# Kernel tuning notes

Measured on AMD Instinct MI355X. Metric: run time of the kernel, lower is better.

## Reference

```python
import jax, jax.numpy as jnp
import numpy as np

SOS_TOKEN = 0
VOCAB, EMBED, HIDDEN = 32000, 256, 256


def setup_inputs() -> dict:
    key = jax.random.key(0)
    ks = jax.random.split(key, 10)
    B, S, T = 32, 128, 128
    s = 0.05
    return {
        "encoder_outputs": jax.random.normal(ks[0], (B, S, HIDDEN), jnp.float32),
        "encoder_hidden": jax.random.normal(ks[1], (1, B, HIDDEN), jnp.float32),
        "target_tensor": jax.random.randint(ks[2], (B, T), 0, VOCAB),
        "embedding": jax.random.normal(ks[3], (VOCAB, EMBED), jnp.float32) * s,
        "W_ih": jax.random.normal(ks[4], (3 * HIDDEN, EMBED + HIDDEN), jnp.float32) * s,
        "W_hh": jax.random.normal(ks[5], (3 * HIDDEN, HIDDEN), jnp.float32) * s,
        "b_ih": jax.random.normal(ks[6], (3 * HIDDEN,), jnp.float32) * s,
        "b_hh": jax.random.normal(ks[7], (3 * HIDDEN,), jnp.float32) * s,
        "W_out": jax.random.normal(ks[8], (VOCAB, HIDDEN), jnp.float32) * s,
        "b_out": jax.random.normal(ks[9], (VOCAB,), jnp.float32) * s,
    }


def _decode(encoder_outputs, encoder_hidden, target_tensor, embedding,
            W_ih, W_hh, b_ih, b_hh, W_out, b_out):
    B, T = target_tensor.shape
    # full teacher forcing: decoder input at step t is target[t-1], step 0 is SOS
    dec_in = jnp.concatenate(
        [jnp.full((B, 1), SOS_TOKEN, dtype=target_tensor.dtype), target_tensor[:, :-1]], axis=1)
    emb = embedding[dec_in]                                     # (B,T,E)
    # attention: query = embedded input, key = value = encoder_outputs
    scores = jnp.einsum("bte,bse->bts", emb, encoder_outputs)   # (B,T,S)
    attn = jax.nn.softmax(scores, axis=2)
    context = jnp.einsum("bts,bsh->bth", attn, encoder_outputs)  # (B,T,H)
    x_seq = jnp.concatenate([emb, context], axis=2)             # (B,T,E+H)
    x_seq = jnp.swapaxes(x_seq, 0, 1)                           # (T,B,E+H)

    def gru_step(h, x):
        gi = x @ W_ih.T + b_ih                                  # (B,3H)
        gh = h @ W_hh.T + b_hh
        i_r, i_z, i_n = jnp.split(gi, 3, axis=1)
        h_r, h_z, h_n = jnp.split(gh, 3, axis=1)
        r = jax.nn.sigmoid(i_r + h_r)
        z = jax.nn.sigmoid(i_z + h_z)
        n = jnp.tanh(i_n + r * h_n)
        h_new = (1.0 - z) * n + z * h
        return h_new, h_new

    h0 = encoder_hidden[0]                                      # (B,H)
    _, hs = jax.lax.scan(gru_step, h0, x_seq)                   # (T,B,H)
    logits = hs @ W_out.T + b_out                               # (T,B,V)
    return jnp.swapaxes(logits, 0, 1)                           # (B,T,V)


def reference(encoder_outputs, encoder_hidden, target_tensor, embedding,
              W_ih, W_hh, b_ih, b_hh, W_out, b_out):
    return _decode(encoder_outputs, encoder_hidden, target_tensor, embedding,
                   W_ih, W_hh, b_ih, b_hh, W_out, b_out)
```

## Files before the change

kernel.cpp:

```cpp
#include <hip/hip_runtime.h>
#include <hip/hip_bf16.h>
#include <stdint.h>

typedef float    f32x4  __attribute__((ext_vector_type(4)));
typedef __bf16   bf16x8 __attribute__((ext_vector_type(8)));
typedef _Float16 f16x8  __attribute__((ext_vector_type(8)));
typedef _Float16 h2v    __attribute__((ext_vector_type(2)));

#define B_ 32
#define S_ 128
#define T_ 128
#define H_ 256
#define E_ 256
#define V_ 32000

__device__ __forceinline__ void gll16(const void* g, void* l) {
  __builtin_amdgcn_global_load_lds(
      (const __attribute__((address_space(1))) uint32_t*)g,
      (__attribute__((address_space(3))) uint32_t*)l,
      16, 0, 0);
}

__device__ __forceinline__ uint32_t pack_pair(float a, float b) {
  unsigned short lo = __builtin_bit_cast(unsigned short, (_Float16)a);
  unsigned short hi = __builtin_bit_cast(unsigned short, (_Float16)b);
  return (uint32_t)lo | ((uint32_t)hi << 16);
}

__device__ __forceinline__ uint32_t pack_bf16(float a, float b) {
  return (uint32_t)__builtin_bit_cast(unsigned short, __float2bfloat16(a)) |
         ((uint32_t)__builtin_bit_cast(unsigned short, __float2bfloat16(b)) << 16);
}

__device__ __forceinline__ float dot2(uint32_t w, uint32_t h, float acc) {
#if __has_builtin(__builtin_amdgcn_fdot2)
  return __builtin_amdgcn_fdot2(__builtin_bit_cast(h2v, w),
                                __builtin_bit_cast(h2v, h), acc, false);
#else
  h2v wv = __builtin_bit_cast(h2v, w);
  h2v hv = __builtin_bit_cast(h2v, h);
  return acc + (float)wv.x * (float)hv.x + (float)wv.y * (float)hv.y;
#endif
}

__device__ __forceinline__ float sigmoid_fast(float x) {
  return __fdividef(1.f, 1.f + __expf(-x));
}
__device__ __forceinline__ float tanh_fast(float x) {
  float e = __expf(2.f * fabsf(x));
  float t = 1.f - __fdividef(2.f, e + 1.f);
  return copysignf(t, x);
}

__global__ __launch_bounds__(256) void cvt_bf16_kernel(
    const float* __restrict__ src, uint32_t* __restrict__ dst, int n) {
  int i = (blockIdx.x * 256 + threadIdx.x) * 8;
  if (i + 7 < n) {
    float4 a = *(const float4*)(src + i);
    float4 b = *(const float4*)(src + i + 4);
    uint4 o;
    o.x = pack_bf16(a.x, a.y);
    o.y = pack_bf16(a.z, a.w);
    o.z = pack_bf16(b.x, b.y);
    o.w = pack_bf16(b.z, b.w);
    *(uint4*)(dst + (i >> 1)) = o;
  }
}

__global__ __launch_bounds__(256) void cvt_f16_kernel(
    const float* __restrict__ src, uint32_t* __restrict__ dst, int n) {
  int i = (blockIdx.x * 256 + threadIdx.x) * 4;
  if (i + 3 < n) {
    float4 v = *(const float4*)(src + i);
    uint2 p;
    p.x = pack_pair(v.x, v.y);
    p.y = pack_pair(v.z, v.w);
    *(uint2*)(dst + (i >> 1)) = p;
  }
}

__global__ __launch_bounds__(256) void pack_whh(
    const float* __restrict__ Whh, uint32_t* __restrict__ Wp) {
  __shared__ float lds[32][257];
  int j0 = blockIdx.x * 32;
  int tid = threadIdx.x;
  #pragma unroll 4
  for (int i = 0; i < 32; ++i)
    lds[i][tid] = Whh[(size_t)(j0 + i) * 256 + tid];
  __syncthreads();
  #pragma unroll 4
  for (int i = 0; i < 16; ++i) {
    int e = i * 256 + tid;
    int k2 = e >> 5;
    int jj = e & 31;
    Wp[(size_t)k2 * 768 + j0 + jj] = pack_pair(lds[jj][2 * k2], lds[jj][2 * k2 + 1]);
  }
}

__global__ __launch_bounds__(256) void attn_kernel(
    const float* __restrict__ enc,
    const int*   __restrict__ tgt,
    const float* __restrict__ embt,
    uint32_t*    __restrict__ xh)
{
  int b   = blockIdx.x;
  int tc  = blockIdx.y;
  int tid = threadIdx.x;
  __shared__ __align__(16) float e_sh[256];
  __shared__ float attn_sh[128];
  __shared__ float red_sh[4];
  const float* encb = enc + (size_t)b * S_ * H_;

  for (int tt = 0; tt < 8; ++tt) {
    int t = tc * 8 + tt;
    int tok = (t == 0) ? 0 : tgt[b * T_ + t - 1];
    float ev = embt[(size_t)tok * E_ + tid];
    e_sh[tid] = ev;
    {
      float other = __shfl_xor(ev, 1);
      if (!(tid & 1))
        xh[(size_t)(t * B_ + b) * 256 + (tid >> 1)] = pack_pair(ev, other);
    }
    __syncthreads();

    float sc = 0.f;
    if (tid < 128) {
      const float* er = encb + tid * H_;
      #pragma unroll 8
      for (int k = 0; k < 256; k += 4) {
        float4 e4 = *(const float4*)(e_sh + k);
        float4 r4 = *(const float4*)(er + k);
        sc += e4.x * r4.x; sc += e4.y * r4.y; sc += e4.z * r4.z; sc += e4.w * r4.w;
      }
      float mx = sc;
      #pragma unroll
      for (int o = 32; o > 0; o >>= 1) mx = fmaxf(mx, __shfl_xor(mx, o, 64));
      if ((tid & 63) == 0) red_sh[tid >> 6] = mx;
    }
    __syncthreads();
    float gmax = fmaxf(red_sh[0], red_sh[1]);
    float p = 0.f;
    if (tid < 128) {
      p = __expf(sc - gmax);
      float s = p;
      #pragma unroll
      for (int o = 32; o > 0; o >>= 1) s += __shfl_xor(s, o, 64);
      if ((tid & 63) == 0) red_sh[2 + (tid >> 6)] = s;
    }
    __syncthreads();
    float tot = red_sh[2] + red_sh[3];
    if (tid < 128) attn_sh[tid] = p / tot;
    __syncthreads();

    float ctx = 0.f;
    #pragma unroll 4
    for (int s = 0; s < 128; ++s) ctx += attn_sh[s] * encb[s * H_ + tid];
    {
      float other = __shfl_xor(ctx, 1);
      if (!(tid & 1))
        xh[(size_t)(t * B_ + b) * 256 + 128 + (tid >> 1)] = pack_pair(ctx, other);
    }
    __syncthreads();
  }
}

__global__ __launch_bounds__(256) void gi_gemm_f16(
    const _Float16* __restrict__ A,
    const _Float16* __restrict__ Bm,
    const float* __restrict__ bih,
    float* __restrict__ gi)
{
  __shared__ _Float16 sA[128 * 64];
  __shared__ _Float16 sB[128 * 64];
  int tid = threadIdx.x;
  int n0 = blockIdx.x * 128;
  int m0 = blockIdx.y * 128;
  int lane = tid & 63;
  int wave = tid >> 6;
  int wm = (wave >> 1) * 64;
  int wn = (wave & 1) * 64;
  int srow = tid >> 3;
  int sk   = (tid & 7) * 8;
  f32x4 acc[4][4] = {};

  for (int kt = 0; kt < 512; kt += 64) {
    #pragma unroll
    for (int it = 0; it < 4; ++it) {
      int row = it * 32 + srow;
      gll16(A  + (size_t)(m0 + row) * 512 + kt + sk, &sA[row * 64 + sk]);
      gll16(Bm + (size_t)(n0 + row) * 512 + kt + sk, &sB[row * 64 + sk]);
    }
    __syncthreads();
    #pragma unroll
    for (int kk = 0; kk < 2; ++kk) {
      f16x8 af[4], bfr[4];
      #pragma unroll
      for (int m = 0; m < 4; ++m)
        af[m] = *(const f16x8*)&sA[(wm + m * 16 + (lane & 15)) * 64 + kk * 32 + (lane >> 4) * 8];
      #pragma unroll
      for (int n = 0; n < 4; ++n)
        bfr[n] = *(const f16x8*)&sB[(wn + n * 16 + (lane & 15)) * 64 + kk * 32 + (lane >> 4) * 8];
      #pragma unroll
      for (int m = 0; m < 4; ++m)
        #pragma unroll
        for (int n = 0; n < 4; ++n)
          acc[m][n] = __builtin_amdgcn_mfma_f32_16x16x32_f16(af[m], bfr[n], acc[m][n], 0, 0, 0);
    }
    __syncthreads();
  }

  #pragma unroll
  for (int n = 0; n < 4; ++n) {
    int col = n0 + wn + n * 16 + (lane & 15);
    float bv = bih[col];
    #pragma unroll
    for (int m = 0; m < 4; ++m) {
      int rbase = m0 + wm + m * 16 + (lane >> 4) * 4;
      #pragma unroll
      for (int r = 0; r < 4; ++r)
        gi[(size_t)(rbase + r) * 768 + col] = acc[m][n][r] + bv;
    }
  }
}

__global__ __launch_bounds__(768) void gru_kernel(
    const float*    __restrict__ gi,
    const uint32_t* __restrict__ Wp,
    const float*    __restrict__ bhh,
    const float*    __restrict__ h0,
    __hip_bfloat16* __restrict__ hs)
{
  int b   = blockIdx.x;
  int tid = threadIdx.x;
  int role = tid >> 8;
  int j    = tid & 255;
  __shared__ __align__(16) uint32_t h2[128];
  __shared__ float r_sh[256];
  __shared__ float z_sh[256];

  uint32_t w[128];
  #pragma unroll
  for (int i = 0; i < 128; ++i) w[i] = Wp[(size_t)i * 768 + tid];
  float bj = bhh[tid];

  float hprev = 0.f;
  if (role == 2) {
    hprev = h0[b * 256 + j];
    float other = __shfl_xor(hprev, 1);
    if (!(j & 1)) h2[j >> 1] = pack_pair(hprev, other);
  }
  float gval = gi[(size_t)b * 768 + tid];
  __syncthreads();

  for (int t = 0; t < 128; ++t) {
    float gnext = 0.f;
    if (t < 127) gnext = gi[(size_t)((t + 1) * 32 + b) * 768 + tid];

    float a0 = 0.f, a1 = 0.f, a2 = 0.f, a3 = 0.f;
    float a4 = 0.f, a5 = 0.f, a6 = 0.f, a7 = 0.f;
    #pragma unroll
    for (int k8 = 0; k8 < 16; ++k8) {
      uint4 ha = *(const uint4*)&h2[k8 * 8];
      uint4 hb = *(const uint4*)&h2[k8 * 8 + 4];
      a0 = dot2(w[k8 * 8 + 0], ha.x, a0);
      a1 = dot2(w[k8 * 8 + 1], ha.y, a1);
      a2 = dot2(w[k8 * 8 + 2], ha.z, a2);
      a3 = dot2(w[k8 * 8 + 3], ha.w, a3);
      a4 = dot2(w[k8 * 8 + 4], hb.x, a4);
      a5 = dot2(w[k8 * 8 + 5], hb.y, a5);
      a6 = dot2(w[k8 * 8 + 6], hb.z, a6);
      a7 = dot2(w[k8 * 8 + 7], hb.w, a7);
    }
    float gh = ((a0 + a1) + (a2 + a3)) + ((a4 + a5) + (a6 + a7)) + bj;

    if (role == 0)      r_sh[j] = sigmoid_fast(gval + gh);
    else if (role == 1) z_sh[j] = sigmoid_fast(gval + gh);
    __syncthreads();

    if (role == 2) {
      float r = r_sh[j];
      float z = z_sh[j];
      float n = tanh_fast(gval + r * gh);
      float hn = (1.f - z) * n + z * hprev;
      hprev = hn;
      hs[(size_t)(t * 32 + b) * 256 + j] = __float2bfloat16(hn);
      float other = __shfl_xor(hn, 1);
      if (!(j & 1)) h2[j >> 1] = pack_pair(hn, other);
    }
    gval = gnext;
    __syncthreads();
  }
}

__global__ __launch_bounds__(256) void logits_gemm(
    const __hip_bfloat16* __restrict__ A,
    const __hip_bfloat16* __restrict__ Bm,
    const float* __restrict__ bout,
    float* __restrict__ out)
{
  __shared__ __hip_bfloat16 sA[128 * 64];
  __shared__ __hip_bfloat16 sB[128 * 64];
  int tid = threadIdx.x;
  int bid = blockIdx.x;
  int chunk = bid & 7;
  int local = bid >> 3;
  int m0 = (chunk * 4 + (local & 3)) * 128;
  int n0 = (local >> 2) * 128;
  int lane = tid & 63;
  int wave = tid >> 6;
  int wm = (wave >> 1) * 64;
  int wn = (wave & 1) * 64;
  int srow = tid >> 3;
  int schunk = tid & 7;
  f32x4 acc[4][4] = {};

  for (int kt = 0; kt < 256; kt += 64) {
    #pragma unroll
    for (int it = 0; it < 4; ++it) {
      int row = it * 32 + srow;
      int gc = ((schunk ^ (row & 7)) * 8);
      gll16(A  + (size_t)(m0 + row) * 256 + kt + gc, &sA[row * 64 + schunk * 8]);
      gll16(Bm + (size_t)(n0 + row) * 256 + kt + gc, &sB[row * 64 + schunk * 8]);
    }
    __syncthreads();
    #pragma unroll
    for (int kk = 0; kk < 2; ++kk) {
      bf16x8 af[4], bfr[4];
      #pragma unroll
      for (int m = 0; m < 4; ++m) {
        int r = wm + m * 16 + (lane & 15);
        int pc = ((kk * 4 + (lane >> 4)) ^ (r & 7)) * 8;
        af[m] = *(const bf16x8*)&sA[r * 64 + pc];
      }
      #pragma unroll
      for (int n = 0; n < 4; ++n) {
        int r = wn + n * 16 + (lane & 15);
        int pc = ((kk * 4 + (lane >> 4)) ^ (r & 7)) * 8;
        bfr[n] = *(const bf16x8*)&sB[r * 64 + pc];
      }
      #pragma unroll
      for (int m = 0; m < 4; ++m)
        #pragma unroll
        for (int n = 0; n < 4; ++n)
          acc[m][n] = __builtin_amdgcn_mfma_f32_16x16x32_bf16(bfr[n], af[m], acc[m][n], 0, 0, 0);
    }
    __syncthreads();
  }

  #pragma unroll
  for (int m = 0; m < 4; ++m) {
    int row = m0 + wm + m * 16 + (lane & 15);
    int t  = row >> 5;
    int bb = row & 31;
    float* orow = out + (size_t)(bb * 128 + t) * 32000;
    #pragma unroll
    for (int n = 0; n < 4; ++n) {
      int col0 = n0 + wn + n * 16 + (lane >> 4) * 4;
      f32x4 bv = *(const f32x4*)&bout[col0];
      f32x4 v = acc[m][n] + bv;
      __builtin_nontemporal_store(v, (f32x4*)&orow[col0]);
    }
  }
}

extern "C" void kernel_launch(void* const* d_in, const int* in_sizes, int n_in,
                              void* d_out, int out_size, void* d_ws, size_t ws_size,
                              hipStream_t stream) {
  const float* enc  = (const float*)d_in[0];
  const float* ench = (const float*)d_in[1];
  const int*   tgt  = (const int*)d_in[2];
  const float* embt = (const float*)d_in[3];
  const float* Wih  = (const float*)d_in[4];
  const float* Whh  = (const float*)d_in[5];
  const float* bih  = (const float*)d_in[6];
  const float* bhh  = (const float*)d_in[7];
  const float* Wout = (const float*)d_in[8];
  const float* bout = (const float*)d_in[9];
  float* out = (float*)d_out;

  char* ws = (char*)d_ws;
  float*          gi    = (float*)(ws);
  __hip_bfloat16* hs    = (__hip_bfloat16*)(ws + 12582912);
  __hip_bfloat16* woutb = (__hip_bfloat16*)(ws + 14680064);
  uint32_t*       xh    = (uint32_t*)(ws + 31064064);
  uint32_t*       wihh  = (uint32_t*)(ws + 35258368);

  uint32_t* Wp = (uint32_t*)(out + ((size_t)out_size - 98304));

  cvt_bf16_kernel<<<4000, 256, 0, stream>>>(Wout, (uint32_t*)woutb, V_ * H_);
  cvt_f16_kernel<<<384, 256, 0, stream>>>(Wih, wihh, 768 * 512);
  pack_whh<<<24, 256, 0, stream>>>(Whh, Wp);
  attn_kernel<<<dim3(32, 16), 256, 0, stream>>>(enc, tgt, embt, xh);
  gi_gemm_f16<<<dim3(6, 32), 256, 0, stream>>>((const _Float16*)xh, (const _Float16*)wihh, bih, gi);
  gru_kernel<<<32, 768, 0, stream>>>(gi, Wp, bhh, ench, hs);
  logits_gemm<<<8000, 256, 0, stream>>>(hs, woutb, bout, out);
}
```

Measured before the change: 471.4 us.

## Fuse GRU recurrence and logits GEMM with flag-based streaming of hidden states

Merges the GRU and output-projection kernels into one launch. The first 32 blocks run the recurrence and publish bf16 hidden states with atomic stores, bumping a per-chunk counter every 4 timesteps. The remaining blocks compute 128x128 logits tiles once their row chunk is ready. This overlaps the serial recurrence with the large vocab GEMM and removes the kernel boundary. The costs are spin-waits, 768-thread blocks where only 256 threads do GEMM work (lower occupancy), and A tiles loaded through scalar atomic loads instead of async LDS loads.

```diff
diff --git a/kernel.cpp b/kernel.cpp
--- a/kernel.cpp
+++ b/kernel.cpp
@@ -50,6 +50,10 @@
   float e = __expf(2.f * fabsf(x));
   float t = 1.f - __fdividef(2.f, e + 1.f);
   return copysignf(t, x);
+}
+
+__global__ __launch_bounds__(512) void zero_flags(uint32_t* flags) {
+  flags[threadIdx.x] = 0;
 }
 
 __global__ __launch_bounds__(256) void cvt_bf16_kernel(
@@ -223,103 +227,132 @@
   }
 }
 
-__global__ __launch_bounds__(768) void gru_kernel(
+__global__ __launch_bounds__(768, 3) void gru_logits(
     const float*    __restrict__ gi,
     const uint32_t* __restrict__ Wp,
     const float*    __restrict__ bhh,
     const float*    __restrict__ h0,
-    __hip_bfloat16* __restrict__ hs)
+    uint32_t*       __restrict__ hsu,
+    const __hip_bfloat16* __restrict__ Bm,
+    const float*    __restrict__ bout,
+    float*          __restrict__ out,
+    uint32_t*       __restrict__ flags)
 {
-  int b   = blockIdx.x;
-  int tid = threadIdx.x;
-  int role = tid >> 8;
-  int j    = tid & 255;
   __shared__ __align__(16) uint32_t h2[128];
   __shared__ float r_sh[256];
   __shared__ float z_sh[256];
-
-  uint32_t w[128];
-  #pragma unroll
-  for (int i = 0; i < 128; ++i) w[i] = Wp[(size_t)i * 768 + tid];
-  float bj = bhh[tid];
-
-  float hprev = 0.f;
-  if (role == 2) {
-    hprev = h0[b * 256 + j];
-    float other = __shfl_xor(hprev, 1);
-    if (!(j & 1)) h2[j >> 1] = pack_pair(hprev, other);
-  }
-  float gval = gi[(size_t)b * 768 + tid];
-  __syncthreads();
-
-  for (int t = 0; t < 128; ++t) {
-    float gnext = 0.f;
-    if (t < 127) gnext = gi[(size_t)((t + 1) * 32 + b) * 768 + tid];
-
-    float a0 = 0.f, a1 = 0.f, a2 = 0.f, a3 = 0.f;
-    float a4 = 0.f, a5 = 0.f, a6 = 0.f, a7 = 0.f;
-    #pragma unroll
-    for (int k8 = 0; k8 < 16; ++k8) {
-      uint4 ha = *(const uint4*)&h2[k8 * 8];
-      uint4 hb = *(const uint4*)&h2[k8 * 8 + 4];
-      a0 = dot2(w[k8 * 8 + 0], ha.x, a0);
-      a1 = dot2(w[k8 * 8 + 1], ha.y, a1);
-      a2 = dot2(w[k8 * 8 + 2], ha.z, a2);
-      a3 = dot2(w[k8 * 8 + 3], ha.w, a3);
-      a4 = dot2(w[k8 * 8 + 4], hb.x, a4);
-      a5 = dot2(w[k8 * 8 + 5], hb.y, a5);
-      a6 = dot2(w[k8 * 8 + 6], hb.z, a6);
-      a7 = dot2(w[k8 * 8 + 7], hb.w, a7);
-    }
-    float gh = ((a0 + a1) + (a2 + a3)) + ((a4 + a5) + (a6 + a7)) + bj;
-
-    if (role == 0)      r_sh[j] = sigmoid_fast(gval + gh);
-    else if (role == 1) z_sh[j] = sigmoid_fast(gval + gh);
-    __syncthreads();
-
+  __shared__ __align__(16) __hip_bfloat16 sA[128 * 64];
+  __shared__ __align__(16) __hip_bfloat16 sB[128 * 64];
+
+  int bid = blockIdx.x;
+  int tid = threadIdx.x;
+
+  if (bid < 32) {
+    int b    = bid;
+    int role = tid >> 8;
+    int j    = tid & 255;
+
+    uint32_t w[128];
+    #pragma unroll
+    for (int i = 0; i < 128; ++i) w[i] = Wp[(size_t)i * 768 + tid];
+    float bj = bhh[tid];
+
+    float hprev = 0.f;
     if (role == 2) {
-      float r = r_sh[j];
-      float z = z_sh[j];
-      float n = tanh_fast(gval + r * gh);
-      float hn = (1.f - z) * n + z * hprev;
-      hprev = hn;
-      hs[(size_t)(t * 32 + b) * 256 + j] = __float2bfloat16(hn);
-      float other = __shfl_xor(hn, 1);
-      if (!(j & 1)) h2[j >> 1] = pack_pair(hn, other);
-    }
-    gval = gnext;
-    __syncthreads();
-  }
-}
-
-__global__ __launch_bounds__(256) void logits_gemm(
-    const __hip_bfloat16* __restrict__ A,
-    const __hip_bfloat16* __restrict__ Bm,
-    const float* __restrict__ bout,
-    float* __restrict__ out)
-{
-  __shared__ __hip_bfloat16 sA[128 * 64];
-  __shared__ __hip_bfloat16 sB[128 * 64];
-  int tid = threadIdx.x;
-  int bid = blockIdx.x;
-  int chunk = bid & 7;
-  int local = bid >> 3;
-  int m0 = (chunk * 4 + (local & 3)) * 128;
-  int n0 = (local >> 2) * 128;
+      hprev = h0[b * 256 + j];
+      float other = __shfl_xor(hprev, 1);
+      if (!(j & 1)) h2[j >> 1] = pack_pair(hprev, other);
+    }
+    float gval = gi[(size_t)b * 768 + tid];
+    __syncthreads();
+
+    for (int t = 0; t < 128; ++t) {
+      float gnext = 0.f;
+      if (t < 127) gnext = gi[(size_t)((t + 1) * 32 + b) * 768 + tid];
+
+      float a0 = 0.f, a1 = 0.f, a2 = 0.f, a3 = 0.f;
+      float a4 = 0.f, a5 = 0.f, a6 = 0.f, a7 = 0.f;
+      #pragma unroll
+      for (int k8 = 0; k8 < 16; ++k8) {
+        uint4 ha = *(const uint4*)&h2[k8 * 8];
+        uint4 hb = *(const uint4*)&h2[k8 * 8 + 4];
+        a0 = dot2(w[k8 * 8 + 0], ha.x, a0);
+        a1 = dot2(w[k8 * 8 + 1], ha.y, a1);
+        a2 = dot2(w[k8 * 8 + 2], ha.z, a2);
+        a3 = dot2(w[k8 * 8 + 3], ha.w, a3);
+        a4 = dot2(w[k8 * 8 + 4], hb.x, a4);
+        a5 = dot2(w[k8 * 8 + 5], hb.y, a5);
+        a6 = dot2(w[k8 * 8 + 6], hb.z, a6);
+        a7 = dot2(w[k8 * 8 + 7], hb.w, a7);
+      }
+      float gh = ((a0 + a1) + (a2 + a3)) + ((a4 + a5) + (a6 + a7)) + bj;
+
+      if (role == 0)      r_sh[j] = sigmoid_fast(gval + gh);
+      else if (role == 1) z_sh[j] = sigmoid_fast(gval + gh);
+      __syncthreads();
+
+      if (role == 2) {
+        float r = r_sh[j];
+        float z = z_sh[j];
+        float n = tanh_fast(gval + r * gh);
+        float hn = (1.f - z) * n + z * hprev;
+        hprev = hn;
+        float other = __shfl_xor(hn, 1);
+        if (!(j & 1)) {
+          h2[j >> 1] = pack_pair(hn, other);
+          __hip_atomic_store(&hsu[(size_t)(t * 32 + b) * 128 + (j >> 1)],
+                             pack_bf16(hn, other),
+                             __ATOMIC_RELAXED, __HIP_MEMORY_SCOPE_AGENT);
+        }
+      }
+      gval = gnext;
+      __syncthreads();
+
+      if ((t & 3) == 3 && tid == 0)
+        __hip_atomic_fetch_add(&flags[(t >> 2) * 16], 1u,
+                               __ATOMIC_RELEASE, __HIP_MEMORY_SCOPE_AGENT);
+    }
+    return;
+  }
+
+  if (tid >= 256) return;
+  int bid2 = bid - 32;
+  int c  = bid2 / 250;
+  int nn = bid2 % 250;
+  int m0 = c * 128;
+  int n0 = nn * 128;
   int lane = tid & 63;
   int wave = tid >> 6;
   int wm = (wave >> 1) * 64;
   int wn = (wave & 1) * 64;
   int srow = tid >> 3;
   int schunk = tid & 7;
+
+  if (tid == 0) {
+    while (__hip_atomic_load(&flags[c * 16], __ATOMIC_ACQUIRE,
+                             __HIP_MEMORY_SCOPE_AGENT) < 32u)
+      __builtin_amdgcn_s_sleep(32);
+  }
+  __syncthreads();
+
+  uint32_t* sAu = (uint32_t*)sA;
   f32x4 acc[4][4] = {};
 
   for (int kt = 0; kt < 256; kt += 64) {
+    #pragma unroll
+    for (int i = 0; i < 16; ++i) {
+      int e = i * 256 + tid;
+      int row = e >> 5;
+      int cu  = e & 31;
+      uint32_t v = __hip_atomic_load(&hsu[(size_t)(m0 + row) * 128 + (kt >> 1) + cu],
+                                     __ATOMIC_RELAXED, __HIP_MEMORY_SCOPE_AGENT);
+      int sc16 = (cu >> 2) ^ (row & 7);
+      sAu[row * 32 + sc16 * 4 + (cu & 3)] = v;
+    }
     #pragma unroll
     for (int it = 0; it < 4; ++it) {
       int row = it * 32 + srow;
       int gc = ((schunk ^ (row & 7)) * 8);
-      gll16(A  + (size_t)(m0 + row) * 256 + kt + gc, &sA[row * 64 + schunk * 8]);
       gll16(Bm + (size_t)(n0 + row) * 256 + kt + gc, &sB[row * 64 + schunk * 8]);
     }
     __syncthreads();
@@ -380,18 +413,19 @@
 
   char* ws = (char*)d_ws;
   float*          gi    = (float*)(ws);
-  __hip_bfloat16* hs    = (__hip_bfloat16*)(ws + 12582912);
+  uint32_t*       hsu   = (uint32_t*)(ws + 12582912);
   __hip_bfloat16* woutb = (__hip_bfloat16*)(ws + 14680064);
   uint32_t*       xh    = (uint32_t*)(ws + 31064064);
   uint32_t*       wihh  = (uint32_t*)(ws + 35258368);
+  uint32_t*       flags = (uint32_t*)(ws + 36044800);
 
   uint32_t* Wp = (uint32_t*)(out + ((size_t)out_size - 98304));
 
+  zero_flags<<<1, 512, 0, stream>>>(flags);
   cvt_bf16_kernel<<<4000, 256, 0, stream>>>(Wout, (uint32_t*)woutb, V_ * H_);
   cvt_f16_kernel<<<384, 256, 0, stream>>>(Wih, wihh, 768 * 512);
   pack_whh<<<24, 256, 0, stream>>>(Whh, Wp);
   attn_kernel<<<dim3(32, 16), 256, 0, stream>>>(enc, tgt, embt, xh);
   gi_gemm_f16<<<dim3(6, 32), 256, 0, stream>>>((const _Float16*)xh, (const _Float16*)wihh, bih, gi);
-  gru_kernel<<<32, 768, 0, stream>>>(gi, Wp, bhh, ench, hs);
-  logits_gemm<<<8000, 256, 0, stream>>>(hs, woutb, bout, out);
-}
+  gru_logits<<<8032, 768, 0, stream>>>(gi, Wp, bhh, ench, hsu, woutb, bout, out, flags);
+}
```

Measured after the change: 729.8 us. +54.8%, slower.
